# Performance work log

Hardware: AMD Instinct MI355X
Metric: run time of the kernel (lower is better)

## Reference

```python
import jax, jax.numpy as jnp
import numpy as np

SR = 16000
HOP = 256
MIN_F0 = 50.0
MAX_F0 = 500.0
MIN_PERIOD = SR // 500          # 32
MAX_PERIOD = SR // 50           # 320
FRAME_LEN = HOP * 2             # 512
LAG_END = min(MAX_PERIOD, FRAME_LEN // 2)  # 256 -> lags 32..255 (224 lags)


def setup_inputs() -> dict:
    key = jax.random.key(0)
    waveform = jax.random.normal(key, (64, 1, 163840), dtype=jnp.float32)
    return {"waveform": waveform}


def reference(waveform):
    B, C, T = waveform.shape
    x = waveform[:, 0, :]  # (B, T)
    pad = FRAME_LEN // 2
    xpad = jnp.pad(x, ((0, 0), (pad, pad)), mode='reflect')
    n_frames = (T + 2 * pad - FRAME_LEN) // HOP + 1  # = T//HOP + 1
    # frame extraction (equivalent to unfold(frame_length, hop))
    idx = np.arange(n_frames)[:, None] * HOP + np.arange(FRAME_LEN)[None, :]
    frames = xpad[:, idx]  # (B, F, L)
    # L2-normalize each frame
    norm = jnp.sqrt(jnp.sum(frames * frames, axis=-1, keepdims=True))
    xn = frames / (norm + 1e-8)
    # zero-pad right so xn[t] * xz[t+p] reproduces frame[:L-p] * frame[p:]
    xz = jnp.pad(xn, ((0, 0), (0, 0), (0, FRAME_LEN)))
    lags = jnp.arange(MIN_PERIOD, LAG_END)

    def step(carry, p):
        sl = jax.lax.dynamic_slice_in_dim(xz, p, FRAME_LEN, axis=-1)
        return carry, jnp.sum(xn * sl, axis=-1)  # (B, F)

    _, ac = jax.lax.scan(step, None, lags)  # (P, B, F)
    max_idx = jnp.argmax(ac, axis=0)  # (B, F)
    period = max_idx.astype(jnp.float32) + MIN_PERIOD
    f0 = SR / (period + 1e-8)
    return jnp.clip(f0, MIN_F0, MAX_F0)  # (B, F)
```

## Files before the change

kernel.cpp:

```cpp
#include <hip/hip_runtime.h>


#define SR_F 16000.0f
#define HOP 256
#define FRAME_LEN 512
#define PAD 256
#define T_LEN 163840
#define N_FRAMES 641
#define MIN_PERIOD 32
#define N_LAGS 224
#define WPB 4
#define NC 15

typedef _Float16 half8 __attribute__((ext_vector_type(8)));
typedef float floatx4 __attribute__((ext_vector_type(4)));
typedef unsigned int uint2v __attribute__((ext_vector_type(2)));

__device__ __forceinline__ int swz(int q) { return q ^ ((q >> 3) & 7); }

__device__ __forceinline__ unsigned int pkh(float a, float b) {
    unsigned short ha = __builtin_bit_cast(unsigned short, (_Float16)a);
    unsigned short hb = __builtin_bit_cast(unsigned short, (_Float16)b);
    return (unsigned int)ha | ((unsigned int)hb << 16);
}

#define DPP_XOR1 0xB1
#define DPP_XOR2 0x4E
#define DPP_ROR4 0x124
#define DPP_ROR8 0x128

template <int CTRL> __device__ __forceinline__ int dppi(int x) {
    return __builtin_amdgcn_update_dpp(0, x, CTRL, 0xF, 0xF, false);
}
template <int CTRL> __device__ __forceinline__ float dppf(float x) {
    return __builtin_bit_cast(float, dppi<CTRL>(__builtin_bit_cast(int, x)));
}

__device__ __forceinline__ uint2v pl16sw(unsigned int x, bool sel) {
#if __has_builtin(__builtin_amdgcn_permlane16_swap)
    (void)sel;
    return __builtin_amdgcn_permlane16_swap(x, x, false, false);
#else
    unsigned int p = (unsigned int)__shfl_xor((int)x, 16);
    uint2v r; r[0] = sel ? p : x; r[1] = sel ? x : p; return r;
#endif
}
__device__ __forceinline__ uint2v pl32sw(unsigned int x, bool sel) {
#if __has_builtin(__builtin_amdgcn_permlane32_swap)
    (void)sel;
    return __builtin_amdgcn_permlane32_swap(x, x, false, false);
#else
    unsigned int p = (unsigned int)__shfl_xor((int)x, 32);
    uint2v r; r[0] = sel ? p : x; r[1] = sel ? x : p; return r;
#endif
}

__device__ __forceinline__ float wave_sum(float x, bool oddrow, bool hihalf) {
    x += dppf<DPP_XOR1>(x);
    x += dppf<DPP_XOR2>(x);
    x += dppf<DPP_ROR4>(x);
    x += dppf<DPP_ROR8>(x);
    uint2v p = pl16sw(__builtin_bit_cast(unsigned int, x), oddrow);
    x = __builtin_bit_cast(float, p[0]) + __builtin_bit_cast(float, p[1]);
    p = pl32sw(__builtin_bit_cast(unsigned int, x), hihalf);
    x = __builtin_bit_cast(float, p[0]) + __builtin_bit_cast(float, p[1]);
    return x;
}

__device__ __forceinline__
void top2_comb(float& v1, int& i1, float& v2, float ov1, int oi1, float ov2) {
    bool take = (ov1 > v1) || (ov1 == v1 && oi1 < i1);
    float lose = take ? v1 : ov1;
    if (take) { v1 = ov1; i1 = oi1; }
    v2 = fmaxf(fmaxf(v2, ov2), lose);
}

template <int CTRL> __device__ __forceinline__
void top2_dpp(float& v1, int& i1, float& v2) {
    float ov1 = dppf<CTRL>(v1);
    int   oi1 = dppi<CTRL>(i1);
    float ov2 = dppf<CTRL>(v2);
    top2_comb(v1, i1, v2, ov1, oi1, ov2);
}

__device__ __forceinline__
void top2_full(floatx4 acc, int qd, int nn, bool oddrow, bool hihalf,
               float& v1, int& i1, float& v2) {
    v1 = acc[0];
    i1 = 64*qd + nn;
    v2 = -__builtin_inff();
    #pragma unroll
    for (int r = 1; r < 4; ++r) {
        float cv = (4*qd + r < 14) ? acc[r] : -__builtin_inff();
        bool take = (cv > v1);
        float lose = take ? v1 : cv;
        if (take) { v1 = cv; i1 = 64*qd + 16*r + nn; }
        v2 = fmaxf(v2, lose);
    }
    top2_dpp<DPP_XOR1>(v1, i1, v2);
    top2_dpp<DPP_XOR2>(v1, i1, v2);
    top2_dpp<DPP_ROR4>(v1, i1, v2);
    top2_dpp<DPP_ROR8>(v1, i1, v2);
    {
        uint2v a = pl16sw(__builtin_bit_cast(unsigned int, v1), oddrow);
        uint2v b = pl16sw((unsigned int)i1, oddrow);
        uint2v c = pl16sw(__builtin_bit_cast(unsigned int, v2), oddrow);
        float ov1 = __builtin_bit_cast(float, oddrow ? a[0] : a[1]);
        int   oi1 = (int)(oddrow ? b[0] : b[1]);
        float ov2 = __builtin_bit_cast(float, oddrow ? c[0] : c[1]);
        top2_comb(v1, i1, v2, ov1, oi1, ov2);
    }
    {
        uint2v a = pl32sw(__builtin_bit_cast(unsigned int, v1), hihalf);
        uint2v b = pl32sw((unsigned int)i1, hihalf);
        uint2v c = pl32sw(__builtin_bit_cast(unsigned int, v2), hihalf);
        float ov1 = __builtin_bit_cast(float, hihalf ? a[0] : a[1]);
        int   oi1 = (int)(hihalf ? b[0] : b[1]);
        float ov2 = __builtin_bit_cast(float, hihalf ? c[0] : c[1]);
        top2_comb(v1, i1, v2, ov1, oi1, ov2);
    }
}

__device__ __forceinline__ void write_copies(unsigned int* e, unsigned int* o,
                                             unsigned int u10, unsigned int u11,
                                             unsigned int u20, unsigned int u21,
                                             int lane) {
    e[120 + 2*lane] = u10;  e[121 + 2*lane] = u11;
    e[248 + 2*lane] = u20;  e[249 + 2*lane] = u21;
    unsigned int a  = __shfl(u10, (lane + 1) & 63);
    unsigned int bb = __shfl(u20, (lane + 1) & 63);
    unsigned int n1 = (lane == 63) ? bb : a;
    unsigned int n2 = (lane == 63) ? 0u : bb;
    o[120 + 2*lane] = (u10 >> 16) | (u11 << 16);
    o[121 + 2*lane] = (u11 >> 16) | (n1 << 16);
    o[248 + 2*lane] = (u20 >> 16) | (u21 << 16);
    o[249 + 2*lane] = (u21 >> 16) | (n2 << 16);
    if (lane == 0) o[119] = u10 << 16;
}

__global__ __launch_bounds__(256, 4) void f0_kernel(const float* __restrict__ wav,
                                                    float* __restrict__ out) {
    __shared__ unsigned int yw[WPB][1600];

    const int tid  = threadIdx.x;
    const int wv   = tid >> 6;
    const int lane = tid & 63;
    unsigned int* ye  = yw[wv];
    unsigned int* yo  = ye + 400;
    unsigned int* le  = ye + 800;
    unsigned int* loo = ye + 1200;

    const int xcd = blockIdx.x & 7;
    const int idx = blockIdx.x >> 3;
    const int bf  = (xcd * 1282 + idx) * WPB + wv;
    const int b   = bf / N_FRAMES;
    const int f   = bf - b * N_FRAMES;
    const float* __restrict__ x = wav + (size_t)b * T_LEN;
    const int base = f * HOP - PAD;
    const bool fast = (f != 0 && f != N_FRAMES - 1);

    const int qd = lane >> 4;
    const int nn = lane & 15;
    const int par = nn & 1;
    const unsigned int* ybh = par ? yo : ye;
    const unsigned int* ybl = par ? loo : le;
    const int wA0 = 120 + 4*qd - 8*nn;
    const int wB0 = 136 + 4*qd + ((nn - par) >> 1);
    const int seg = lane & 15;
    const bool s0 = (seg & 1), s1 = (seg & 2), s2 = (seg & 4), s3 = (seg & 8);
    const bool oddrow = (lane & 16) != 0;
    const bool hihalf = (lane & 32) != 0;

    float4 c1, c2;
    if (fast) {
        const float4* g4 = (const float4*)(x + base);
        c1 = g4[lane];
        c2 = g4[lane + 64];
    }
    ye[lane] = 0u; yo[lane] = 0u;
    if (lane < 56) { ye[64 + lane] = 0u; yo[64 + lane] = 0u; }
    if (lane < 25) { ye[375 + lane] = 0u; yo[375 + lane] = 0u; }

    float qen = 0.0f;
    if (fast) {
        qen = c1.x*c1.x + c1.y*c1.y + c1.z*c1.z + c1.w*c1.w
            + c2.x*c2.x + c2.y*c2.y + c2.z*c2.z + c2.w*c2.w;
        write_copies(ye, yo, pkh(c1.x, c1.y), pkh(c1.z, c1.w),
                             pkh(c2.x, c2.y), pkh(c2.z, c2.w), lane);
    } else {
        for (int t = lane; t < FRAME_LEN; t += 64) {
            int idxr = base + t;
            if (idxr < 0) idxr = -idxr;
            if (idxr >= T_LEN) idxr = 2 * (T_LEN - 1) - idxr;
            float v = x[idxr];
            qen = __builtin_fmaf(v, v, qen);
            unsigned short h = __builtin_bit_cast(unsigned short, (_Float16)v);
            ((unsigned short*)ye)[240 + t] = h;
            ((unsigned short*)yo)[239 + t] = h;
        }
    }
    __threadfence_block();

    qen = wave_sum(qen, oddrow, hihalf);

    floatx4 acc0 = {0.f, 0.f, 0.f, 0.f};
    floatx4 acc1 = {0.f, 0.f, 0.f, 0.f};
    #pragma unroll
    for (int c = 0; c < NC; ++c) {
        uint4 au = *(const uint4*)(ye + (wA0 + 16*c));
        const unsigned int* pb = ybh + (wB0 + 16*c);
        uint4 bu; bu.x = pb[0]; bu.y = pb[1]; bu.z = pb[2]; bu.w = pb[3];
        if (c & 1)
            acc1 = __builtin_amdgcn_mfma_f32_16x16x32_f16(
                __builtin_bit_cast(half8, au), __builtin_bit_cast(half8, bu),
                acc1, 0, 0, 0);
        else
            acc0 = __builtin_amdgcn_mfma_f32_16x16x32_f16(
                __builtin_bit_cast(half8, au), __builtin_bit_cast(half8, bu),
                acc0, 0, 0, 0);
    }
    floatx4 acc = acc0 + acc1;

    float v1, v2; int i1;
    top2_full(acc, qd, nn, oddrow, hihalf, v1, i1, v2);

    const float E1 = 9.765625e-4f * qen + 0.05f;
    if (v1 - v2 > 2.0f * E1) {
        if (lane == 0) {
            float period = (float)(i1 + MIN_PERIOD);
            float f0 = SR_F / (period + 1e-8f);
            out[bf] = fminf(fmaxf(f0, 50.0f), 500.0f);
        }
        return;
    }

    le[lane] = 0u; loo[lane] = 0u;
    if (lane < 56) { le[64 + lane] = 0u; loo[64 + lane] = 0u; }
    if (lane < 25) { le[375 + lane] = 0u; loo[375 + lane] = 0u; }
    if (fast) {
        float l0 = c1.x - (float)(_Float16)c1.x;
        float l1 = c1.y - (float)(_Float16)c1.y;
        float l2 = c1.z - (float)(_Float16)c1.z;
        float l3 = c1.w - (float)(_Float16)c1.w;
        float l4 = c2.x - (float)(_Float16)c2.x;
        float l5 = c2.y - (float)(_Float16)c2.y;
        float l6 = c2.z - (float)(_Float16)c2.z;
        float l7 = c2.w - (float)(_Float16)c2.w;
        write_copies(le, loo, pkh(l0, l1), pkh(l2, l3),
                              pkh(l4, l5), pkh(l6, l7), lane);
    } else {
        for (int t = lane; t < FRAME_LEN; t += 64) {
            int idxr = base + t;
            if (idxr < 0) idxr = -idxr;
            if (idxr >= T_LEN) idxr = 2 * (T_LEN - 1) - idxr;
            float v = x[idxr];
            float l = v - (float)(_Float16)v;
            unsigned short h = __builtin_bit_cast(unsigned short, (_Float16)l);
            ((unsigned short*)le)[240 + t] = h;
            ((unsigned short*)loo)[239 + t] = h;
        }
    }
    __threadfence_block();

    #pragma unroll
    for (int c = 0; c < NC; ++c) {
        uint4 au = *(const uint4*)(ye + (wA0 + 16*c));
        const unsigned int* p = ybl + (wB0 + 16*c);
        uint4 bu; bu.x = p[0]; bu.y = p[1]; bu.z = p[2]; bu.w = p[3];
        acc = __builtin_amdgcn_mfma_f32_16x16x32_f16(
            __builtin_bit_cast(half8, au), __builtin_bit_cast(half8, bu),
            acc, 0, 0, 0);
    }
    #pragma unroll
    for (int c = 0; c < NC; ++c) {
        uint4 au = *(const uint4*)(le + (wA0 + 16*c));
        const unsigned int* p = ybh + (wB0 + 16*c);
        uint4 bu; bu.x = p[0]; bu.y = p[1]; bu.z = p[2]; bu.w = p[3];
        acc = __builtin_amdgcn_mfma_f32_16x16x32_f16(
            __builtin_bit_cast(half8, au), __builtin_bit_cast(half8, bu),
            acc, 0, 0, 0);
    }

    top2_full(acc, qd, nn, oddrow, hihalf, v1, i1, v2);

    const float E2 = 1.0e-4f * qen + 0.02f;
    if (v1 - v2 > 2.0f * E2) {
        if (lane == 0) {
            float period = (float)(i1 + MIN_PERIOD);
            float f0 = SR_F / (period + 1e-8f);
            out[bf] = fminf(fmaxf(f0, 50.0f), 500.0f);
        }
        return;
    }

    float* sw = (float*)ye;
    if (fast) {
        const float4* g4 = (const float4*)(x + base);
        ((float4*)sw)[swz(lane)]      = g4[lane];
        ((float4*)sw)[swz(lane + 64)] = g4[lane + 64];
        if (lane < 16) ((float4*)sw)[swz(lane + 128)] = make_float4(0.f,0.f,0.f,0.f);
    } else {
        for (int t = lane; t < FRAME_LEN; t += 64) {
            int idxr = base + t;
            if (idxr < 0) idxr = -idxr;
            if (idxr >= T_LEN) idxr = 2 * (T_LEN - 1) - idxr;
            sw[(swz(t >> 2) << 2) | (t & 3)] = x[idxr];
        }
        int t = FRAME_LEN + lane;
        sw[(swz(t >> 2) << 2) | (t & 3)] = 0.0f;
    }
    __threadfence_block();

    const float4* s4 = (const float4*)sw;
    double dtot[4];
    #pragma unroll
    for (int r = 0; r < 4; ++r) {
        const int g  = (r << 2) + qd;
        const int p0 = MIN_PERIOD + (g << 4);
        double dacc[16];
        #pragma unroll
        for (int j = 0; j < 16; ++j) dacc[j] = 0.0;
        if (g < 14) {
            const int n16 = (FRAME_LEN - p0 + 15) >> 4;
            #pragma unroll
            for (int k = 0; k < 2; ++k) {
                const int ch = seg + (k << 4);
                if (ch < n16) {
                    const int t  = ch << 4;
                    const int qa = t >> 2;
                    const int qw = (t + p0) >> 2;
                    float a[16], w[32];
                    #pragma unroll
                    for (int u = 0; u < 4; ++u) {
                        float4 v = s4[swz(qa + u)];
                        a[4*u+0]=v.x; a[4*u+1]=v.y; a[4*u+2]=v.z; a[4*u+3]=v.w;
                    }
                    #pragma unroll
                    for (int u = 0; u < 8; ++u) {
                        float4 v = s4[swz(qw + u)];
                        w[4*u+0]=v.x; w[4*u+1]=v.y; w[4*u+2]=v.z; w[4*u+3]=v.w;
                    }
                    #pragma unroll
                    for (int j = 0; j < 16; ++j) {
                        #pragma unroll
                        for (int i = 0; i < 16; ++i)
                            dacc[j] = fma((double)a[i], (double)w[i + j], dacc[j]);
                    }
                }
            }
        }
        double u8[8], u4[4], u2[2], dtotal;
        #pragma unroll
        for (int i = 0; i < 8; ++i) {
            double lo = dacc[2*i], hi = dacc[2*i+1];
            double keep = s0 ? hi : lo, send = s0 ? lo : hi;
            u8[i] = keep + __shfl_xor(send, 1);
        }
        #pragma unroll
        for (int i = 0; i < 4; ++i) {
            double lo = u8[2*i], hi = u8[2*i+1];
            double keep = s1 ? hi : lo, send = s1 ? lo : hi;
            u4[i] = keep + __shfl_xor(send, 2);
        }
        #pragma unroll
        for (int i = 0; i < 2; ++i) {
            double lo = u4[2*i], hi = u4[2*i+1];
            double keep = s2 ? hi : lo, send = s2 ? lo : hi;
            u2[i] = keep + __shfl_xor(send, 4);
        }
        {
            double lo = u2[0], hi = u2[1];
            double keep = s3 ? hi : lo, send = s3 ? lo : hi;
            dtotal = keep + __shfl_xor(send, 8);
        }
        dtot[r] = ((r << 6) + lane < N_LAGS) ? dtotal : -__builtin_inf();
    }
    double dv1 = dtot[0];
    int    di1 = lane;
    #pragma unroll
    for (int r = 1; r < 4; ++r) {
        double c = dtot[r];
        if (c > dv1) { dv1 = c; di1 = (r << 6) + lane; }
    }
    #pragma unroll
    for (int m = 1; m < 64; m <<= 1) {
        double o = __shfl_xor(dv1, m);
        int   oi = __shfl_xor(di1, m);
        if (o > dv1 || (o == dv1 && oi < di1)) { dv1 = o; di1 = oi; }
    }
    if (lane == 0) {
        float period = (float)(di1 + MIN_PERIOD);
        float f0 = SR_F / (period + 1e-8f);
        out[bf] = fminf(fmaxf(f0, 50.0f), 500.0f);
    }
}

extern "C" void kernel_launch(void* const* d_in, const int* in_sizes, int n_in,
                              void* d_out, int out_size, void* d_ws, size_t ws_size,
                              hipStream_t stream) {
    const float* wav = (const float*)d_in[0];
    float* out = (float*)d_out;
    const int n_blocks = (64 * N_FRAMES) / WPB;
    f0_kernel<<<n_blocks, 256, 0, stream>>>(wav, out);
}
```

Before: 130.2 us.

## Process two frames per wavefront to interleave MFMA chains and halve block count

Each wavefront now handles two frames, one from each half of the frame range. Their loads, fp16 packing, and first-pass MFMA correlation are interleaved, so the two independent MFMA chains can hide each other's latency. Frames that fail the cheap margin test are then refined serially through a factored-out helper. LDS per block doubles to 3200 words per wave, which may lower occupancy, and the serial fallback path adds divergence when only one of the two frames needs refinement.

```diff
diff --git a/kernel.cpp b/kernel.cpp
--- a/kernel.cpp
+++ b/kernel.cpp
@@ -7,6 +7,8 @@
 #define PAD 256
 #define T_LEN 163840
 #define N_FRAMES 641
+#define TOTAL (64 * N_FRAMES)
+#define HALF (TOTAL / 2)
 #define MIN_PERIOD 32
 #define N_LAGS 224
 #define WPB 4
@@ -138,101 +140,23 @@
     if (lane == 0) o[119] = u10 << 16;
 }
 
-__global__ __launch_bounds__(256, 4) void f0_kernel(const float* __restrict__ wav,
-                                                    float* __restrict__ out) {
-    __shared__ unsigned int yw[WPB][1600];
-
-    const int tid  = threadIdx.x;
-    const int wv   = tid >> 6;
-    const int lane = tid & 63;
-    unsigned int* ye  = yw[wv];
-    unsigned int* yo  = ye + 400;
-    unsigned int* le  = ye + 800;
-    unsigned int* loo = ye + 1200;
-
-    const int xcd = blockIdx.x & 7;
-    const int idx = blockIdx.x >> 3;
-    const int bf  = (xcd * 1282 + idx) * WPB + wv;
-    const int b   = bf / N_FRAMES;
-    const int f   = bf - b * N_FRAMES;
-    const float* __restrict__ x = wav + (size_t)b * T_LEN;
-    const int base = f * HOP - PAD;
-    const bool fast = (f != 0 && f != N_FRAMES - 1);
-
-    const int qd = lane >> 4;
-    const int nn = lane & 15;
-    const int par = nn & 1;
+__device__ __forceinline__ void emit(float* out, int bf, int i1) {
+    float period = (float)(i1 + MIN_PERIOD);
+    float f0 = SR_F / (period + 1e-8f);
+    out[bf] = fminf(fmaxf(f0, 50.0f), 500.0f);
+}
+
+__device__ __forceinline__ void finish_frame(
+    const float* __restrict__ x, int base, bool fast, int bf,
+    float* __restrict__ out,
+    unsigned int* ye, unsigned int* yo, unsigned int* le, unsigned int* loo,
+    float4 c1, float4 c2, floatx4 acc, float qen, int lane,
+    int qd, int nn, int par, int wA0, int wB0, int seg,
+    bool oddrow, bool hihalf) {
+
     const unsigned int* ybh = par ? yo : ye;
     const unsigned int* ybl = par ? loo : le;
-    const int wA0 = 120 + 4*qd - 8*nn;
-    const int wB0 = 136 + 4*qd + ((nn - par) >> 1);
-    const int seg = lane & 15;
     const bool s0 = (seg & 1), s1 = (seg & 2), s2 = (seg & 4), s3 = (seg & 8);
-    const bool oddrow = (lane & 16) != 0;
-    const bool hihalf = (lane & 32) != 0;
-
-    float4 c1, c2;
-    if (fast) {
-        const float4* g4 = (const float4*)(x + base);
-        c1 = g4[lane];
-        c2 = g4[lane + 64];
-    }
-    ye[lane] = 0u; yo[lane] = 0u;
-    if (lane < 56) { ye[64 + lane] = 0u; yo[64 + lane] = 0u; }
-    if (lane < 25) { ye[375 + lane] = 0u; yo[375 + lane] = 0u; }
-
-    float qen = 0.0f;
-    if (fast) {
-        qen = c1.x*c1.x + c1.y*c1.y + c1.z*c1.z + c1.w*c1.w
-            + c2.x*c2.x + c2.y*c2.y + c2.z*c2.z + c2.w*c2.w;
-        write_copies(ye, yo, pkh(c1.x, c1.y), pkh(c1.z, c1.w),
-                             pkh(c2.x, c2.y), pkh(c2.z, c2.w), lane);
-    } else {
-        for (int t = lane; t < FRAME_LEN; t += 64) {
-            int idxr = base + t;
-            if (idxr < 0) idxr = -idxr;
-            if (idxr >= T_LEN) idxr = 2 * (T_LEN - 1) - idxr;
-            float v = x[idxr];
-            qen = __builtin_fmaf(v, v, qen);
-            unsigned short h = __builtin_bit_cast(unsigned short, (_Float16)v);
-            ((unsigned short*)ye)[240 + t] = h;
-            ((unsigned short*)yo)[239 + t] = h;
-        }
-    }
-    __threadfence_block();
-
-    qen = wave_sum(qen, oddrow, hihalf);
-
-    floatx4 acc0 = {0.f, 0.f, 0.f, 0.f};
-    floatx4 acc1 = {0.f, 0.f, 0.f, 0.f};
-    #pragma unroll
-    for (int c = 0; c < NC; ++c) {
-        uint4 au = *(const uint4*)(ye + (wA0 + 16*c));
-        const unsigned int* pb = ybh + (wB0 + 16*c);
-        uint4 bu; bu.x = pb[0]; bu.y = pb[1]; bu.z = pb[2]; bu.w = pb[3];
-        if (c & 1)
-            acc1 = __builtin_amdgcn_mfma_f32_16x16x32_f16(
-                __builtin_bit_cast(half8, au), __builtin_bit_cast(half8, bu),
-                acc1, 0, 0, 0);
-        else
-            acc0 = __builtin_amdgcn_mfma_f32_16x16x32_f16(
-                __builtin_bit_cast(half8, au), __builtin_bit_cast(half8, bu),
-                acc0, 0, 0, 0);
-    }
-    floatx4 acc = acc0 + acc1;
-
-    float v1, v2; int i1;
-    top2_full(acc, qd, nn, oddrow, hihalf, v1, i1, v2);
-
-    const float E1 = 9.765625e-4f * qen + 0.05f;
-    if (v1 - v2 > 2.0f * E1) {
-        if (lane == 0) {
-            float period = (float)(i1 + MIN_PERIOD);
-            float f0 = SR_F / (period + 1e-8f);
-            out[bf] = fminf(fmaxf(f0, 50.0f), 500.0f);
-        }
-        return;
-    }
 
     le[lane] = 0u; loo[lane] = 0u;
     if (lane < 56) { le[64 + lane] = 0u; loo[64 + lane] = 0u; }
@@ -281,15 +205,12 @@
             acc, 0, 0, 0);
     }
 
+    float v1, v2; int i1;
     top2_full(acc, qd, nn, oddrow, hihalf, v1, i1, v2);
 
     const float E2 = 1.0e-4f * qen + 0.02f;
     if (v1 - v2 > 2.0f * E2) {
-        if (lane == 0) {
-            float period = (float)(i1 + MIN_PERIOD);
-            float f0 = SR_F / (period + 1e-8f);
-            out[bf] = fminf(fmaxf(f0, 50.0f), 500.0f);
-        }
+        if (lane == 0) emit(out, bf, i1);
         return;
     }
 
@@ -388,11 +309,159 @@
         int   oi = __shfl_xor(di1, m);
         if (o > dv1 || (o == dv1 && oi < di1)) { dv1 = o; di1 = oi; }
     }
-    if (lane == 0) {
-        float period = (float)(di1 + MIN_PERIOD);
-        float f0 = SR_F / (period + 1e-8f);
-        out[bf] = fminf(fmaxf(f0, 50.0f), 500.0f);
-    }
+    if (lane == 0) emit(out, bf, di1);
+}
+
+__global__ __launch_bounds__(256, 4) void f0_kernel(const float* __restrict__ wav,
+                                                    float* __restrict__ out) {
+    __shared__ unsigned int yw[WPB][3200];
+
+    const int tid  = threadIdx.x;
+    const int wv   = tid >> 6;
+    const int lane = tid & 63;
+    unsigned int* yeA = yw[wv];
+    unsigned int* yoA = yeA + 400;
+    unsigned int* leA = yeA + 800;
+    unsigned int* loA = yeA + 1200;
+    unsigned int* yeB = yeA + 1600;
+    unsigned int* yoB = yeA + 2000;
+    unsigned int* leB = yeA + 2400;
+    unsigned int* loB = yeA + 2800;
+
+    const int xcd = blockIdx.x & 7;
+    const int idx = blockIdx.x >> 3;
+    const int bfA = (xcd * 641 + idx) * WPB + wv;
+    const int bfB = bfA + HALF;
+    const int bA  = bfA / N_FRAMES;
+    const int fA  = bfA - bA * N_FRAMES;
+    const int bB  = bfB / N_FRAMES;
+    const int fB  = bfB - bB * N_FRAMES;
+    const float* __restrict__ xA = wav + (size_t)bA * T_LEN;
+    const float* __restrict__ xB = wav + (size_t)bB * T_LEN;
+    const int baseA = fA * HOP - PAD;
+    const int baseB = fB * HOP - PAD;
+    const bool fastA = (fA != 0 && fA != N_FRAMES - 1);
+    const bool fastB = (fB != 0 && fB != N_FRAMES - 1);
+
+    const int qd = lane >> 4;
+    const int nn = lane & 15;
+    const int par = nn & 1;
+    const int wA0 = 120 + 4*qd - 8*nn;
+    const int wB0 = 136 + 4*qd + ((nn - par) >> 1);
+    const int seg = lane & 15;
+    const bool oddrow = (lane & 16) != 0;
+    const bool hihalf = (lane & 32) != 0;
+
+    float4 cA1, cA2, cB1, cB2;
+    if (fastA) {
+        const float4* g4 = (const float4*)(xA + baseA);
+        cA1 = g4[lane];
+        cA2 = g4[lane + 64];
+    }
+    if (fastB) {
+        const float4* g4 = (const float4*)(xB + baseB);
+        cB1 = g4[lane];
+        cB2 = g4[lane + 64];
+    }
+    yeA[lane] = 0u; yoA[lane] = 0u; yeB[lane] = 0u; yoB[lane] = 0u;
+    if (lane < 56) { yeA[64+lane]=0u; yoA[64+lane]=0u; yeB[64+lane]=0u; yoB[64+lane]=0u; }
+    if (lane < 25) { yeA[375+lane]=0u; yoA[375+lane]=0u; yeB[375+lane]=0u; yoB[375+lane]=0u; }
+
+    float qenA = 0.0f, qenB = 0.0f;
+    if (fastA) {
+        qenA = cA1.x*cA1.x + cA1.y*cA1.y + cA1.z*cA1.z + cA1.w*cA1.w
+             + cA2.x*cA2.x + cA2.y*cA2.y + cA2.z*cA2.z + cA2.w*cA2.w;
+        write_copies(yeA, yoA, pkh(cA1.x, cA1.y), pkh(cA1.z, cA1.w),
+                               pkh(cA2.x, cA2.y), pkh(cA2.z, cA2.w), lane);
+    } else {
+        for (int t = lane; t < FRAME_LEN; t += 64) {
+            int idxr = baseA + t;
+            if (idxr < 0) idxr = -idxr;
+            if (idxr >= T_LEN) idxr = 2 * (T_LEN - 1) - idxr;
+            float v = xA[idxr];
+            qenA = __builtin_fmaf(v, v, qenA);
+            unsigned short h = __builtin_bit_cast(unsigned short, (_Float16)v);
+            ((unsigned short*)yeA)[240 + t] = h;
+            ((unsigned short*)yoA)[239 + t] = h;
+        }
+    }
+    if (fastB) {
+        qenB = cB1.x*cB1.x + cB1.y*cB1.y + cB1.z*cB1.z + cB1.w*cB1.w
+             + cB2.x*cB2.x + cB2.y*cB2.y + cB2.z*cB2.z + cB2.w*cB2.w;
+        write_copies(yeB, yoB, pkh(cB1.x, cB1.y), pkh(cB1.z, cB1.w),
+                               pkh(cB2.x, cB2.y), pkh(cB2.z, cB2.w), lane);
+    } else {
+        for (int t = lane; t < FRAME_LEN; t += 64) {
+            int idxr = baseB + t;
+            if (idxr < 0) idxr = -idxr;
+            if (idxr >= T_LEN) idxr = 2 * (T_LEN - 1) - idxr;
+            float v = xB[idxr];
+            qenB = __builtin_fmaf(v, v, qenB);
+            unsigned short h = __builtin_bit_cast(unsigned short, (_Float16)v);
+            ((unsigned short*)yeB)[240 + t] = h;
+            ((unsigned short*)yoB)[239 + t] = h;
+        }
+    }
+    __threadfence_block();
+
+    qenA = wave_sum(qenA, oddrow, hihalf);
+    qenB = wave_sum(qenB, oddrow, hihalf);
+
+    const unsigned int* ybhA = par ? yoA : yeA;
+    const unsigned int* ybhB = par ? yoB : yeB;
+    floatx4 aA0 = {0.f,0.f,0.f,0.f}, aA1 = {0.f,0.f,0.f,0.f};
+    floatx4 aB0 = {0.f,0.f,0.f,0.f}, aB1 = {0.f,0.f,0.f,0.f};
+    #pragma unroll
+    for (int c = 0; c < NC; ++c) {
+        uint4 auA = *(const uint4*)(yeA + (wA0 + 16*c));
+        const unsigned int* pA = ybhA + (wB0 + 16*c);
+        uint4 buA; buA.x = pA[0]; buA.y = pA[1]; buA.z = pA[2]; buA.w = pA[3];
+        uint4 auB = *(const uint4*)(yeB + (wA0 + 16*c));
+        const unsigned int* pB = ybhB + (wB0 + 16*c);
+        uint4 buB; buB.x = pB[0]; buB.y = pB[1]; buB.z = pB[2]; buB.w = pB[3];
+        if (c & 1) {
+            aA1 = __builtin_amdgcn_mfma_f32_16x16x32_f16(
+                __builtin_bit_cast(half8, auA), __builtin_bit_cast(half8, buA),
+                aA1, 0, 0, 0);
+            aB1 = __builtin_amdgcn_mfma_f32_16x16x32_f16(
+                __builtin_bit_cast(half8, auB), __builtin_bit_cast(half8, buB),
+                aB1, 0, 0, 0);
+        } else {
+            aA0 = __builtin_amdgcn_mfma_f32_16x16x32_f16(
+                __builtin_bit_cast(half8, auA), __builtin_bit_cast(half8, buA),
+                aA0, 0, 0, 0);
+            aB0 = __builtin_amdgcn_mfma_f32_16x16x32_f16(
+                __builtin_bit_cast(half8, auB), __builtin_bit_cast(half8, buB),
+                aB0, 0, 0, 0);
+        }
+    }
+    floatx4 accA = aA0 + aA1;
+    floatx4 accB = aB0 + aB1;
+
+    float v1A, v2A; int i1A;
+    top2_full(accA, qd, nn, oddrow, hihalf, v1A, i1A, v2A);
+    float v1B, v2B; int i1B;
+    top2_full(accB, qd, nn, oddrow, hihalf, v1B, i1B, v2B);
+
+    const float E1A = 9.765625e-4f * qenA + 0.05f;
+    const float E1B = 9.765625e-4f * qenB + 0.05f;
+    const bool okA = (v1A - v2A > 2.0f * E1A);
+    const bool okB = (v1B - v2B > 2.0f * E1B);
+
+    if (okA) {
+        if (lane == 0) emit(out, bfA, i1A);
+    }
+    if (okB) {
+        if (lane == 0) emit(out, bfB, i1B);
+    }
+    if (!okA)
+        finish_frame(xA, baseA, fastA, bfA, out, yeA, yoA, leA, loA,
+                     cA1, cA2, accA, qenA, lane, qd, nn, par, wA0, wB0,
+                     seg, oddrow, hihalf);
+    if (!okB)
+        finish_frame(xB, baseB, fastB, bfB, out, yeB, yoB, leB, loB,
+                     cB1, cB2, accB, qenB, lane, qd, nn, par, wA0, wB0,
+                     seg, oddrow, hihalf);
 }
 
 extern "C" void kernel_launch(void* const* d_in, const int* in_sizes, int n_in,
@@ -400,6 +469,6 @@
                               hipStream_t stream) {
     const float* wav = (const float*)d_in[0];
     float* out = (float*)d_out;
-    const int n_blocks = (64 * N_FRAMES) / WPB;
+    const int n_blocks = HALF / WPB;
     f0_kernel<<<n_blocks, 256, 0, stream>>>(wav, out);
 }
```

After: 149.1 us. +14.5%, slower.
